# Performance work log

Measured on AMD Instinct MI355X. Metric: run time of the kernel, lower is better.

The kernel has to match this reference:

```python
import jax, jax.numpy as jnp
import numpy as np


def setup_inputs() -> dict:
    key = jax.random.key(0)
    ks = jax.random.split(key, 5)
    B, S, H = 4, 4096, 512
    std = 1.0 / np.sqrt(H)
    x = jax.random.normal(ks[0], (B, S, H), dtype=jnp.float32)
    relative_pos = jax.random.normal(ks[1], (B, S, H), dtype=jnp.float32)
    Wq = jax.random.normal(ks[2], (H, H), dtype=jnp.float32) * std
    Wk = jax.random.normal(ks[3], (H, H), dtype=jnp.float32) * std
    Wv = jax.random.normal(ks[4], (H, H), dtype=jnp.float32) * std
    bq = jnp.zeros((H,), dtype=jnp.float32)
    bk = jnp.zeros((H,), dtype=jnp.float32)
    bv = jnp.zeros((H,), dtype=jnp.float32)
    return {"x": x, "relative_pos": relative_pos, "Wq": Wq, "bq": bq,
            "Wk": Wk, "bk": bk, "Wv": Wv, "bv": bv}


def reference(x, relative_pos, Wq, bq, Wk, bk, Wv, bv):
    H = x.shape[-1]
    scale = jnp.sqrt(jnp.asarray(H, dtype=x.dtype))
    # torch Linear: y = x @ W^T + b
    Q = jnp.einsum('bsh,oh->bso', x, Wq) + bq
    K = jnp.einsum('bsh,oh->bso', x, Wk) + bk
    V = jnp.einsum('bsh,oh->bso', x, Wv) + bv
    Kr = jnp.einsum('bsh,oh->bso', relative_pos, Wk) + bk
    # two score terms, each [B,S,S]
    scores = (jnp.einsum('bqd,bkd->bqk', Q, K) +
              jnp.einsum('bqd,bkd->bqk', Q, Kr)) / scale
    weights = jax.nn.softmax(scores, axis=-1)
    return jnp.einsum('bqk,bkd->bqd', weights, V)
```

## Files before the change

### kernel.cpp

```cpp
#include <hip/hip_runtime.h>
#include <stdint.h>

typedef __attribute__((ext_vector_type(8))) short bf16x8;
typedef __attribute__((ext_vector_type(4))) float f32x4;

#define AS1 __attribute__((address_space(1)))
#define AS3 __attribute__((address_space(3)))

__device__ __forceinline__ void gl2lds16(const void* g, void* l) {
    __builtin_amdgcn_global_load_lds((const AS1 void*)g, (AS3 void*)l, 16, 0, 0);
}

__device__ __forceinline__ unsigned short f2bf(float f) {
    uint32_t u = __builtin_bit_cast(uint32_t, f);
    uint32_t r = (u + 0x7fffu + ((u >> 16) & 1u)) >> 16;
    return (unsigned short)r;
}

constexpr int S = 4096;
constexpr int H = 512;
constexpr size_t OFF_XB  = 0;
constexpr size_t OFF_SB  = 16777216;
constexpr size_t OFF_WQB = 33554432;
constexpr size_t OFF_WKB = 34078720;
constexpr size_t OFF_WVB = 34603008;
constexpr size_t OFF_BQK = 35127296;
constexpr size_t OFF_QB  = 35131392;
constexpr size_t OFF_K2B = OFF_QB  + 16777216;
constexpr size_t OFF_VTB = OFF_K2B + 16777216;
constexpr size_t OFF_PB  = OFF_VTB + 16777216;
constexpr size_t OFF_L   = OFF_PB  + 134217728;

__global__ __launch_bounds__(256) void prep_all(const float* __restrict__ x,
                                                const float* __restrict__ rp,
                                                const float* __restrict__ wq,
                                                const float* __restrict__ wk,
                                                const float* __restrict__ wv,
                                                const float* __restrict__ bq,
                                                const float* __restrict__ bk,
                                                unsigned short* __restrict__ xb,
                                                unsigned short* __restrict__ sb,
                                                unsigned short* __restrict__ wqb,
                                                unsigned short* __restrict__ wkb,
                                                unsigned short* __restrict__ wvb,
                                                float* __restrict__ bqk,
                                                float* __restrict__ lrow) {
    if (blockIdx.x < 8192) {
        const int i = (blockIdx.x * 256 + threadIdx.x) * 4;
        float4 xv = *(const float4*)(x + i);
        float4 rv = *(const float4*)(rp + i);
        uint2 xo, so;
        xo.x = (uint32_t)f2bf(xv.x) | ((uint32_t)f2bf(xv.y) << 16);
        xo.y = (uint32_t)f2bf(xv.z) | ((uint32_t)f2bf(xv.w) << 16);
        so.x = (uint32_t)f2bf(xv.x + rv.x) | ((uint32_t)f2bf(xv.y + rv.y) << 16);
        so.y = (uint32_t)f2bf(xv.z + rv.z) | ((uint32_t)f2bf(xv.w + rv.w) << 16);
        *(uint2*)(xb + i) = xo;
        *(uint2*)(sb + i) = so;
    } else {
        const int t = (blockIdx.x - 8192) * 256 + threadIdx.x;
        const int i = t * 4;
        float4 q = *(const float4*)(wq + i);
        float4 k = *(const float4*)(wk + i);
        float4 v = *(const float4*)(wv + i);
        uint2 o;
        o.x = (uint32_t)f2bf(q.x) | ((uint32_t)f2bf(q.y) << 16);
        o.y = (uint32_t)f2bf(q.z) | ((uint32_t)f2bf(q.w) << 16);
        *(uint2*)(wqb + i) = o;
        o.x = (uint32_t)f2bf(k.x) | ((uint32_t)f2bf(k.y) << 16);
        o.y = (uint32_t)f2bf(k.z) | ((uint32_t)f2bf(k.w) << 16);
        *(uint2*)(wkb + i) = o;
        o.x = (uint32_t)f2bf(v.x) | ((uint32_t)f2bf(v.y) << 16);
        o.y = (uint32_t)f2bf(v.z) | ((uint32_t)f2bf(v.w) << 16);
        *(uint2*)(wvb + i) = o;
        if (t < 128) {
            *(float4*)(bqk + t * 4) = *(const float4*)(bq + t * 4);
        } else if (t < 256) {
            const int u = t - 128;
            float4 b = *(const float4*)(bk + u * 4);
            *(float4*)(bqk + 512 + u * 4) = make_float4(2.f * b.x, 2.f * b.y, 2.f * b.z, 2.f * b.w);
        }
        if (t < 4096) {
            *(float4*)(lrow + t * 4) = make_float4(0.f, 0.f, 0.f, 0.f);
        }
    }
}

template <int MODE, int SWZ, int NPANEL>
__global__ __launch_bounds__(256, 2)
void gemm_bt(const unsigned short* __restrict__ Abase,
             const unsigned short* __restrict__ Bbase,
             void* __restrict__ Cbase,
             int M, int N, int K,
             long long sAz, long long sBz, long long sCz,
             const float* __restrict__ bias_n, long long sBNz,
             const float* __restrict__ bias_m,
             float scale,
             float* __restrict__ rowdiv, long long sRz)
{
    int bx = blockIdx.x, by = blockIdx.y, bz = blockIdx.z;
    if (SWZ) {
        const int gx = gridDim.x, gy = gridDim.y;
        const int id  = bx + gx * (by + gridDim.y * bz);
        const int xcd = id & 7;
        const int k   = id >> 3;
        const int kg  = k / gx;
        bx = k - kg * gx;
        const int g = xcd + 8 * kg;
        const int gz = g / gy;
        by = g - gz * gy;
        bz = gz;
    }
    const int z = bz;
    const unsigned short* A  = Abase + (size_t)z * (size_t)sAz;
    const unsigned short* Bm = Bbase + (size_t)z * (size_t)sBz;
    const int bn = bx * 128;
    const int bm = by * 128;

    constexpr int STAGE_BYTES = NPANEL * 16384;
    constexpr int SMEM_BYTES = (MODE == 1) ? STAGE_BYTES
                             : (STAGE_BYTES > 34816 ? STAGE_BYTES : 34816);
    __shared__ __align__(16) char smem[SMEM_BYTES];
    unsigned short* As = (unsigned short*)smem;
    unsigned short* Bs = (unsigned short*)(smem + NPANEL * 8192);

    const int tid  = threadIdx.x;
    const int wave = tid >> 6;
    const int lane = tid & 63;
    const int lm   = lane & 15;
    const int quad = lane >> 4;
    const int wm   = (wave >> 1) * 64;
    const int wn   = (wave & 1) * 64;

    const int r0 = tid >> 2;
    const int p0 = tid & 3;

    f32x4 acc[4][4] = {};

    for (int k0 = 0; k0 < K; k0 += 32 * NPANEL) {
        __syncthreads();
        #pragma unroll
        for (int pp = 0; pp < NPANEL; pp++) {
            const unsigned short* Ap = A  + (size_t)(bm + r0) * K + k0 + pp * 32 + p0 * 8;
            const unsigned short* Bp = Bm + (size_t)(bn + r0) * K + k0 + pp * 32 + p0 * 8;
            unsigned short* Asp = As + pp * 4096;
            unsigned short* Bsp = Bs + pp * 4096;
            gl2lds16(Ap,                    Asp + wave * 512);
            gl2lds16(Ap + (size_t)64 * K,   Asp + 2048 + wave * 512);
            gl2lds16(Bp,                    Bsp + wave * 512);
            gl2lds16(Bp + (size_t)64 * K,   Bsp + 2048 + wave * 512);
        }
        __syncthreads();

        #pragma unroll
        for (int pp = 0; pp < NPANEL; pp++) {
            bf16x8 af[4], bfr[4];
            #pragma unroll
            for (int t = 0; t < 4; t++)
                af[t]  = *(const bf16x8*)(As + pp * 4096 + (wm + t * 16 + lm) * 32 + quad * 8);
            #pragma unroll
            for (int t = 0; t < 4; t++)
                bfr[t] = *(const bf16x8*)(Bs + pp * 4096 + (wn + t * 16 + lm) * 32 + quad * 8);
            #pragma unroll
            for (int mt = 0; mt < 4; mt++)
                #pragma unroll
                for (int nt = 0; nt < 4; nt++)
                    acc[mt][nt] = __builtin_amdgcn_mfma_f32_16x16x32_bf16(af[mt], bfr[nt], acc[mt][nt], 0, 0, 0);
        }
    }

    if (MODE == 1) {
        float* C = (float*)Cbase + (size_t)z * (size_t)sCz;
        const float* rd = rowdiv + (size_t)z * (size_t)sRz;
        #pragma unroll
        for (int mt = 0; mt < 4; mt++) {
            #pragma unroll
            for (int i = 0; i < 4; i++) {
                const int row = bm + wm + mt * 16 + quad * 4 + i;
                const float inv = 1.0f / rd[row];
                const size_t rb = (size_t)row * (size_t)N;
                #pragma unroll
                for (int nt = 0; nt < 4; nt++) {
                    const int col = bn + wn + nt * 16 + lm;
                    C[rb + col] = acc[mt][nt][i] * inv;
                }
            }
        }
    } else {
        unsigned short* C = (unsigned short*)Cbase + (size_t)z * (size_t)sCz;
        const float* bn_ptr = (MODE == 0 && bias_n) ? bias_n + (size_t)z * (size_t)sBNz : nullptr;
        float* lr = (MODE == 2) ? rowdiv + (size_t)z * (size_t)sRz : nullptr;
        unsigned short* Ct = (unsigned short*)smem;
        __syncthreads();
        #pragma unroll
        for (int mt = 0; mt < 4; mt++) {
            #pragma unroll
            for (int i = 0; i < 4; i++) {
                const int r = wm + mt * 16 + quad * 4 + i;
                if (MODE == 0) {
                    const float badd = bias_m ? bias_m[bm + r] : 0.0f;
                    #pragma unroll
                    for (int nt = 0; nt < 4; nt++) {
                        const int col = bn + wn + nt * 16 + lm;
                        float v = acc[mt][nt][i] * scale + badd;
                        if (bn_ptr) v += bn_ptr[col];
                        Ct[r * 136 + wn + nt * 16 + lm] = f2bf(v);
                    }
                } else {
                    float rsum = 0.f;
                    #pragma unroll
                    for (int nt = 0; nt < 4; nt++) {
                        float p = __expf(acc[mt][nt][i] * scale);
                        rsum += p;
                        Ct[r * 136 + wn + nt * 16 + lm] = f2bf(p);
                    }
                    rsum += __shfl_xor(rsum, 1);
                    rsum += __shfl_xor(rsum, 2);
                    rsum += __shfl_xor(rsum, 4);
                    rsum += __shfl_xor(rsum, 8);
                    if (lm == 0) atomicAdd(lr + bm + r, rsum);
                }
            }
        }
        __syncthreads();
        #pragma unroll
        for (int j = 0; j < 8; j++) {
            const int r   = (tid >> 4) + 16 * j;
            const int c16 = tid & 15;
            uint4 vv = *(const uint4*)(Ct + r * 136 + c16 * 8);
            *(uint4*)(C + (size_t)(bm + r) * (size_t)N + bn + c16 * 8) = vv;
        }
    }
}

extern "C" void kernel_launch(void* const* d_in, const int* in_sizes, int n_in,
                              void* d_out, int out_size, void* d_ws, size_t ws_size,
                              hipStream_t stream) {
    const float* x  = (const float*)d_in[0];
    const float* rp = (const float*)d_in[1];
    const float* Wq = (const float*)d_in[2];
    const float* bq = (const float*)d_in[3];
    const float* Wk = (const float*)d_in[4];
    const float* bk = (const float*)d_in[5];
    const float* Wv = (const float*)d_in[6];
    const float* bv = (const float*)d_in[7];

    char* ws = (char*)d_ws;
    unsigned short* xb  = (unsigned short*)(ws + OFF_XB);
    unsigned short* sb  = (unsigned short*)(ws + OFF_SB);
    unsigned short* wqb = (unsigned short*)(ws + OFF_WQB);
    unsigned short* wkb = (unsigned short*)(ws + OFF_WKB);
    unsigned short* wvb = (unsigned short*)(ws + OFF_WVB);
    float*          bqk = (float*)(ws + OFF_BQK);
    unsigned short* qb  = (unsigned short*)(ws + OFF_QB);
    unsigned short* k2b = (unsigned short*)(ws + OFF_K2B);
    unsigned short* vtb = (unsigned short*)(ws + OFF_VTB);
    unsigned short* pb  = (unsigned short*)(ws + OFF_PB);
    float*          lrow = (float*)(ws + OFF_L);

    prep_all<<<8448, 256, 0, stream>>>(x, rp, Wq, Wk, Wv, bq, bk,
                                       xb, sb, wqb, wkb, wvb, bqk, lrow);

    gemm_bt<0, 1, 2><<<dim3(4, 128, 2), 256, 0, stream>>>(
        xb, wqb, qb, 16384, 512, 512,
        8388608, 262144, 8388608,
        bqk, 512, nullptr, 1.0f, nullptr, 0);
    gemm_bt<0, 0, 2><<<dim3(32, 4, 4), 256, 0, stream>>>(
        wvb, xb, vtb, 512, 4096, 512,
        0, (long long)S * H, (long long)S * H,
        nullptr, 0, bv, 1.0f, nullptr, 0);
    gemm_bt<2, 0, 2><<<dim3(32, 32, 4), 256, 0, stream>>>(
        qb, k2b, pb, 4096, 4096, 512,
        (long long)S * H, (long long)S * H, (long long)S * S,
        nullptr, 0, nullptr, 0.044194173824159216f,
        lrow, 4096);
    gemm_bt<1, 1, 4><<<dim3(4, 32, 4), 256, 0, stream>>>(
        pb, vtb, d_out, 4096, 512, 4096,
        (long long)S * S, (long long)S * H, (long long)S * H,
        nullptr, 0, nullptr, 1.0f, lrow, 4096);
}
```

Before: 352.8 us.

## Replace QK^T exp GEMM with 256x256 8-wave double-buffered pipelined kernel

Replaces the generic gemm_bt used for the QK^T score plus exp stage with a dedicated kernel. It uses 256x256 output tiles across 8 waves and double-buffered swizzled LDS staging via global_load_lds, and interleaves loads with MFMA phases using barriers and setprio. Blocks are remapped so neighbouring tiles land on the same XCD for L2 reuse. The larger tiles cut global re-reads of Q and K, but they use 128KB of LDS and many accumulator registers, which limits occupancy and makes the hand-written schedule sensitive to tuning.

```diff
diff --git a/kernel.cpp b/kernel.cpp
--- a/kernel.cpp
+++ b/kernel.cpp
@@ -232,6 +232,181 @@
     }
 }
 
+__global__ __launch_bounds__(512, 2)
+void qk_exp_8ph(const unsigned short* __restrict__ Qb,
+                const unsigned short* __restrict__ K2b,
+                unsigned short* __restrict__ Pb,
+                float* __restrict__ lrow)
+{
+    constexpr int N  = 4096;
+    constexpr int Kd = 512;
+    constexpr float scale = 0.044194173824159216f;
+    __shared__ __align__(16) char smem8[131072];
+
+    int bx = blockIdx.x, by = blockIdx.y, bz = blockIdx.z;
+    {
+        const int gx = gridDim.x, gy = gridDim.y;
+        const int id  = bx + gx * (by + gy * bz);
+        const int xcd = id & 7;
+        const int k   = id >> 3;
+        const int kg  = k / gx;
+        bx = k - kg * gx;
+        const int g = xcd + 8 * kg;
+        const int gz = g / gy;
+        by = g - gz * gy;
+        bz = gz;
+    }
+    const int z  = bz;
+    const int bm = by * 256;
+    const int bn = bx * 256;
+    const unsigned short* Az = Qb  + (size_t)z * (size_t)N * Kd;
+    const unsigned short* Bz = K2b + (size_t)z * (size_t)N * Kd;
+
+    unsigned short* A0 = (unsigned short*)smem8;
+    unsigned short* B0 = A0 + 256 * 64;
+    unsigned short* A1 = B0 + 256 * 64;
+    unsigned short* B1 = A1 + 256 * 64;
+
+    const int tid  = threadIdx.x;
+    const int wave = tid >> 6;
+    const int lane = tid & 63;
+    const int lm   = lane & 15;
+    const int quad = lane >> 4;
+    const int r2   = wave >> 2;
+    const int c4   = wave & 3;
+
+    const int srcslot = (lane & 7) ^ ((lane >> 3) & 7);
+    const unsigned short* aSt = Az + (size_t)(bm + wave * 16 + (lane >> 3)) * Kd + srcslot * 8;
+    const unsigned short* bSt = Bz + (size_t)(bn + wave * 16 + (lane >> 3)) * Kd + srcslot * 8;
+    unsigned short* aLd0 = A0 + wave * 16 * 64;
+    unsigned short* bLd0 = B0 + wave * 16 * 64;
+    unsigned short* aLd1 = A1 + wave * 16 * 64;
+    unsigned short* bLd1 = B1 + wave * 16 * 64;
+
+#define STG(gbase, ld, t, h) { \
+    gl2lds16((gbase) + (h) * 128 * Kd + (t) * 64,          (ld) + (h) * 128 * 64); \
+    gl2lds16((gbase) + (h) * 128 * Kd + 8 * Kd + (t) * 64, (ld) + (h) * 128 * 64 + 8 * 64); }
+
+    f32x4 acc[2][2][4][2] = {};
+    bf16x8 af[4][2], bf0[2][2], bf1[2][2];
+
+#define LD_AF(Abuf, HM) { _Pragma("unroll") for (int m = 0; m < 4; ++m) { \
+      const int row_ = (HM) * 128 + r2 * 64 + m * 16 + lm; \
+      const char* rp_ = (const char*)(Abuf) + row_ * 128; \
+      const int sw_ = (row_ & 7) << 4; \
+      af[m][0] = *(const bf16x8*)(rp_ + ((quad * 16) ^ sw_)); \
+      af[m][1] = *(const bf16x8*)(rp_ + ((64 + quad * 16) ^ sw_)); } }
+
+#define LD_BF(dst, Bbuf, HN) { _Pragma("unroll") for (int n = 0; n < 2; ++n) { \
+      const int row_ = (HN) * 128 + c4 * 32 + n * 16 + lm; \
+      const char* rp_ = (const char*)(Bbuf) + row_ * 128; \
+      const int sw_ = (row_ & 7) << 4; \
+      dst[n][0] = *(const bf16x8*)(rp_ + ((quad * 16) ^ sw_)); \
+      dst[n][1] = *(const bf16x8*)(rp_ + ((64 + quad * 16) ^ sw_)); } }
+
+#define MM(HM, HN, BF) { _Pragma("unroll") for (int m = 0; m < 4; ++m) \
+      _Pragma("unroll") for (int n = 0; n < 2; ++n) \
+      _Pragma("unroll") for (int ks = 0; ks < 2; ++ks) \
+        acc[HM][HN][m][n] = __builtin_amdgcn_mfma_f32_16x16x32_bf16(af[m][ks], BF[n][ks], acc[HM][HN][m][n], 0, 0, 0); }
+
+#define BAR_MFMA(HM, HN, BF) \
+    __builtin_amdgcn_s_barrier(); \
+    asm volatile("s_waitcnt lgkmcnt(0)" ::: "memory"); \
+    __builtin_amdgcn_sched_barrier(0); \
+    __builtin_amdgcn_s_setprio(1); \
+    MM(HM, HN, BF); \
+    __builtin_amdgcn_s_setprio(0);
+
+    STG(aSt, aLd0, 0, 0); STG(aSt, aLd0, 0, 1);
+    STG(bSt, bLd0, 0, 0); STG(bSt, bLd0, 0, 1);
+    STG(aSt, aLd1, 1, 0);
+    STG(bSt, bLd1, 1, 0);
+    asm volatile("s_waitcnt vmcnt(4)" ::: "memory");
+    __builtin_amdgcn_s_barrier();
+
+    #pragma unroll
+    for (int i = 0; i < 4; ++i) {
+        const int t1 = 2 * i + 1, t2 = 2 * i + 2, t3 = 2 * i + 3;
+        LD_AF(A0, 0); LD_BF(bf0, B0, 0);
+        STG(aSt, aLd1, t1, 1); STG(bSt, bLd1, t1, 1);
+        BAR_MFMA(0, 0, bf0);
+        __builtin_amdgcn_s_barrier();
+        LD_BF(bf1, B0, 1);
+        BAR_MFMA(0, 1, bf1);
+        __builtin_amdgcn_s_barrier();
+        LD_AF(A0, 1);
+        if (t2 < 8) STG(aSt, aLd0, t2, 0);
+        BAR_MFMA(1, 0, bf0);
+        __builtin_amdgcn_s_barrier();
+        if (t2 < 8) STG(bSt, bLd0, t2, 0);
+        BAR_MFMA(1, 1, bf1);
+        if (i == 3) { asm volatile("s_waitcnt vmcnt(0)" ::: "memory"); }
+        else        { asm volatile("s_waitcnt vmcnt(4)" ::: "memory"); }
+        __builtin_amdgcn_s_barrier();
+        LD_AF(A1, 0); LD_BF(bf0, B1, 0);
+        if (t2 < 8) { STG(aSt, aLd0, t2, 1); STG(bSt, bLd0, t2, 1); }
+        BAR_MFMA(0, 0, bf0);
+        __builtin_amdgcn_s_barrier();
+        LD_BF(bf1, B1, 1);
+        BAR_MFMA(0, 1, bf1);
+        __builtin_amdgcn_s_barrier();
+        LD_AF(A1, 1);
+        if (t3 < 8) STG(aSt, aLd1, t3, 0);
+        BAR_MFMA(1, 0, bf0);
+        __builtin_amdgcn_s_barrier();
+        if (t3 < 8) STG(bSt, bLd1, t3, 0);
+        BAR_MFMA(1, 1, bf1);
+        asm volatile("s_waitcnt vmcnt(4)" ::: "memory");
+        __builtin_amdgcn_s_barrier();
+    }
+
+    asm volatile("" ::: "memory");
+    unsigned short* Ct = (unsigned short*)smem8;
+    float* lr = lrow + (size_t)z * 4096;
+    unsigned short* Cz = Pb + (size_t)z * (size_t)N * N;
+
+    #pragma unroll
+    for (int hm = 0; hm < 2; ++hm)
+    #pragma unroll
+    for (int m = 0; m < 4; ++m)
+    #pragma unroll
+    for (int i2 = 0; i2 < 4; ++i2) {
+        const int row = hm * 128 + r2 * 64 + m * 16 + quad * 4 + i2;
+        char* rowp = (char*)Ct + row * 512;
+        const int sw = (row & 7) << 4;
+        float rs = 0.f;
+        #pragma unroll
+        for (int hn = 0; hn < 2; ++hn)
+        #pragma unroll
+        for (int n = 0; n < 2; ++n) {
+            const float p = __expf(acc[hm][hn][m][n][i2] * scale);
+            rs += p;
+            const int col = hn * 128 + c4 * 32 + n * 16 + lm;
+            *(unsigned short*)(rowp + ((col * 2) ^ sw)) = f2bf(p);
+        }
+        rs += __shfl_xor(rs, 1);
+        rs += __shfl_xor(rs, 2);
+        rs += __shfl_xor(rs, 4);
+        rs += __shfl_xor(rs, 8);
+        if (lm == 0) atomicAdd(lr + bm + row, rs);
+    }
+    asm volatile("s_waitcnt lgkmcnt(0)" ::: "memory");
+    __builtin_amdgcn_s_barrier();
+    __builtin_amdgcn_sched_barrier(0);
+    #pragma unroll
+    for (int j = 0; j < 16; ++j) {
+        const int row = j * 16 + (tid >> 5);
+        const int cg  = tid & 31;
+        const uint4 v = *(const uint4*)((const char*)Ct + row * 512 + ((cg * 16) ^ ((row & 7) << 4)));
+        *(uint4*)(Cz + (size_t)(bm + row) * N + bn + cg * 8) = v;
+    }
+#undef STG
+#undef LD_AF
+#undef LD_BF
+#undef MM
+#undef BAR_MFMA
+}
+
 extern "C" void kernel_launch(void* const* d_in, const int* in_sizes, int n_in,
                               void* d_out, int out_size, void* d_ws, size_t ws_size,
                               hipStream_t stream) {
@@ -268,11 +443,7 @@
         wvb, xb, vtb, 512, 4096, 512,
         0, (long long)S * H, (long long)S * H,
         nullptr, 0, bv, 1.0f, nullptr, 0);
-    gemm_bt<2, 0, 2><<<dim3(32, 32, 4), 256, 0, stream>>>(
-        qb, k2b, pb, 4096, 4096, 512,
-        (long long)S * H, (long long)S * H, (long long)S * S,
-        nullptr, 0, nullptr, 0.044194173824159216f,
-        lrow, 4096);
+    qk_exp_8ph<<<dim3(16, 16, 4), 512, 0, stream>>>(qb, k2b, pb, lrow);
     gemm_bt<1, 1, 4><<<dim3(4, 32, 4), 256, 0, stream>>>(
         pb, vtb, d_out, 4096, 512, 4096,
         (long long)S * S, (long long)S * H, (long long)S * H,
```

After: 357.2 us. No clear change (+1.2%).
